# Optimization experiments

Hardware: AMD Instinct MI355X
Metric: run time of the kernel (lower is better)

## Reference

```python
import jax, jax.numpy as jnp
import numpy as np

B, S, E, H = 4, 2048, 1024, 16
D = E // H  # head dim = 64


def setup_inputs() -> dict:
    key = jax.random.key(0)
    ks = jax.random.split(key, 9)
    s_in = 1.0 / np.sqrt(E)
    return {
        "x": jax.random.normal(ks[0], (B, S, E), dtype=jnp.float32),
        # stacked per-head projection weights, acting as x @ W + b
        "Wq": jax.random.normal(ks[1], (H, E, D), dtype=jnp.float32) * s_in,
        "bq": jax.random.normal(ks[2], (H, D), dtype=jnp.float32) * 0.01,
        "Wk": jax.random.normal(ks[3], (H, E, D), dtype=jnp.float32) * s_in,
        "bk": jax.random.normal(ks[4], (H, D), dtype=jnp.float32) * 0.01,
        "Wv": jax.random.normal(ks[5], (H, E, D), dtype=jnp.float32) * s_in,
        "bv": jax.random.normal(ks[6], (H, D), dtype=jnp.float32) * 0.01,
        "Wo": jax.random.normal(ks[7], (E, E), dtype=jnp.float32) * s_in,
        "bo": jax.random.normal(ks[8], (E,), dtype=jnp.float32) * 0.01,
    }


def reference(x, Wq, bq, Wk, bk, Wv, bv, Wo, bo):
    # Batched per-head projections (equivalent to the per-head nn.Linear loop)
    q = jnp.einsum("bse,hed->bhsd", x, Wq) + bq[None, :, None, :]
    k = jnp.einsum("bse,hed->bhsd", x, Wk) + bk[None, :, None, :]
    v = jnp.einsum("bse,hed->bhsd", x, Wv) + bv[None, :, None, :]
    scale = 1.0 / jnp.sqrt(jnp.asarray(D, dtype=x.dtype))
    scores = jnp.einsum("bhsd,bhtd->bhst", q, k) * scale  # [B,H,S,S]
    attn = jax.nn.softmax(scores, axis=-1)
    ctx = jnp.einsum("bhst,bhtd->bhsd", attn, v)  # [B,H,S,D]
    # torch.cat over heads along last dim -> [B,S,H*D]=[B,S,E]
    ctx = jnp.transpose(ctx, (0, 2, 1, 3)).reshape(x.shape[0], x.shape[1], E)
    return ctx @ Wo + bo
```

## Files before the change

### kernel.cpp

```cpp
#include <hip/hip_runtime.h>
#include <math.h>

#define B_ 4
#define S_ 2048
#define E_ 1024
#define H_ 16
#define D_ 64
#define BH_ (B_ * H_)

#define SCALE_LOG2E 0.18033688011112042f

typedef short short8 __attribute__((ext_vector_type(8)));
typedef float f32x4 __attribute__((ext_vector_type(4)));
typedef float f32x16 __attribute__((ext_vector_type(16)));

static __device__ __forceinline__ unsigned short f2bf(float f) {
    unsigned int u = __float_as_uint(f);
    unsigned int r = (u + 0x7fffu + ((u >> 16) & 1u)) >> 16;
    return (unsigned short)r;
}

static __device__ __forceinline__ unsigned int pack_bf16_trunc(float hi, float lo) {
    return __builtin_amdgcn_perm(__float_as_uint(hi), __float_as_uint(lo), 0x07060302u);
}

static __device__ __forceinline__ void gl_lds16(const unsigned short* g, unsigned short* l) {
    __builtin_amdgcn_global_load_lds(
        (const __attribute__((address_space(1))) unsigned int*)g,
        (__attribute__((address_space(3))) unsigned int*)l, 16, 0, 0);
}


__global__ __launch_bounds__(256) void xcvt_kernel(
    const float* __restrict__ x, unsigned short* __restrict__ Xb)
{
    size_t i = ((size_t)blockIdx.x * 256 + threadIdx.x) * 8;
    float4 a = *(const float4*)&x[i];
    float4 b = *(const float4*)&x[i + 4];
    ushort4 u0, u1;
    u0.x = f2bf(a.x); u0.y = f2bf(a.y); u0.z = f2bf(a.z); u0.w = f2bf(a.w);
    u1.x = f2bf(b.x); u1.y = f2bf(b.y); u1.z = f2bf(b.z); u1.w = f2bf(b.w);
    *(ushort4*)&Xb[i]     = u0;
    *(ushort4*)&Xb[i + 4] = u1;
}

__global__ __launch_bounds__(256) void wtrans_qkv_kernel(
    const float* __restrict__ Wq, const float* __restrict__ Wk,
    const float* __restrict__ Wv, unsigned short* __restrict__ Wt)
{
    __shared__ float t[32][33];
    const int tx = threadIdx.x & 31, ty = threadIdx.x >> 5;
    const int r0 = blockIdx.x * 32, c0 = blockIdx.y * 32;
    const int z = blockIdx.z, mtx = z >> 4, h = z & 15;
    const float* s = (mtx == 0 ? Wq : (mtx == 1 ? Wk : Wv)) + (size_t)h * E_ * D_;
    const float scale = (mtx == 0) ? SCALE_LOG2E : 1.0f;
    unsigned short* d = Wt + (size_t)mtx * E_ * E_ + (size_t)h * D_ * E_;
#pragma unroll
    for (int i = 0; i < 4; ++i)
        t[ty + i * 8][tx] = s[(size_t)(r0 + ty + i * 8) * D_ + c0 + tx];
    __syncthreads();
#pragma unroll
    for (int i = 0; i < 4; ++i)
        d[(size_t)(c0 + ty + i * 8) * E_ + r0 + tx] = f2bf(t[tx][ty + i * 8] * scale);
}

__global__ __launch_bounds__(256) void wtrans_kernel(
    const float* __restrict__ src, unsigned short* __restrict__ dst, int R, int C)
{
    __shared__ float t[32][33];
    const int tx = threadIdx.x & 31, ty = threadIdx.x >> 5;
    const int r0 = blockIdx.x * 32, c0 = blockIdx.y * 32;
#pragma unroll
    for (int i = 0; i < 4; ++i)
        t[ty + i * 8][tx] = src[(size_t)(r0 + ty + i * 8) * C + c0 + tx];
    __syncthreads();
#pragma unroll
    for (int i = 0; i < 4; ++i)
        dst[(size_t)(c0 + ty + i * 8) * R + r0 + tx] = f2bf(t[tx][ty + i * 8]);
}

__global__ __launch_bounds__(256, 4) void qkv_gemm_kernel(
    const unsigned short* __restrict__ Xb, const unsigned short* __restrict__ Wt,
    const float* __restrict__ bq, const float* __restrict__ bk,
    const float* __restrict__ bv,
    unsigned short* __restrict__ Qh, unsigned short* __restrict__ Kh,
    unsigned short* __restrict__ Vth)
{
    __shared__ unsigned short As[2][128 * 32];
    __shared__ unsigned short Bs[2][128 * 32];
    const int tid = threadIdx.x;
    const int lane = tid & 63, wid = tid >> 6;
    const int quad = lane >> 4, lc = lane & 15;
    const int wm = wid >> 1, wn = wid & 1;
    const int m0 = blockIdx.y * 128, n0 = blockIdx.x * 128;
    const int srow = lane >> 2;
    const int sch  = (((lane & 3) ^ ((lane >> 2) & 3) ^ ((lane >> 4) & 3))) * 8;
    const int swzr = (lc & 3) ^ ((lc >> 2) & 3);

    f32x4 acc[4][4];
#pragma unroll
    for (int mt = 0; mt < 4; ++mt)
#pragma unroll
        for (int nt = 0; nt < 4; ++nt)
            acc[mt][nt] = (f32x4){0.f, 0.f, 0.f, 0.f};

#pragma unroll
    for (int i = 0; i < 2; ++i) {
        int rw = wid * 32 + i * 16;
        gl_lds16(&Xb[(size_t)(m0 + rw + srow) * E_ + sch], &As[0][rw * 32]);
        gl_lds16(&Wt[(size_t)(n0 + rw + srow) * E_ + sch], &Bs[0][rw * 32]);
    }
    __syncthreads();

    for (int k0 = 0; k0 < E_; k0 += 32) {
        const int cur = (k0 >> 5) & 1;
        if (k0 + 32 < E_) {
#pragma unroll
            for (int i = 0; i < 2; ++i) {
                int rw = wid * 32 + i * 16;
                gl_lds16(&Xb[(size_t)(m0 + rw + srow) * E_ + k0 + 32 + sch], &As[cur ^ 1][rw * 32]);
                gl_lds16(&Wt[(size_t)(n0 + rw + srow) * E_ + k0 + 32 + sch], &Bs[cur ^ 1][rw * 32]);
            }
        }
        short8 a[4], bfr[4];
#pragma unroll
        for (int mt = 0; mt < 4; ++mt)
            a[mt] = *(const short8*)&As[cur][(wm * 64 + mt * 16 + lc) * 32 +
                                            ((quad ^ swzr) << 3)];
#pragma unroll
        for (int nt = 0; nt < 4; ++nt)
            bfr[nt] = *(const short8*)&Bs[cur][(wn * 64 + nt * 16 + lc) * 32 +
                                              ((quad ^ swzr) << 3)];
#pragma unroll
        for (int mt = 0; mt < 4; ++mt)
#pragma unroll
            for (int nt = 0; nt < 4; ++nt)
                acc[mt][nt] = __builtin_amdgcn_mfma_f32_16x16x32_bf16(
                    a[mt], bfr[nt], acc[mt][nt], 0, 0, 0);
        __syncthreads();
    }

    const int nb = n0 + wn * 64;
    const int mtx = nb >> 10;
    const int h = (nb >> 6) & 15;
    const int sg0 = m0 + wm * 64;
    const int bb_ = sg0 >> 11;
    const int bhv = bb_ * H_ + h;
    if (mtx < 2) {
        const float bsc = (mtx == 0) ? SCALE_LOG2E : 1.0f;
        const float* bias = (mtx == 0 ? bq : bk) + h * D_;
        unsigned short* Out = (mtx == 0) ? Qh : Kh;
        const size_t obase = (size_t)bhv * (S_ / 32) * 2048;
#pragma unroll
        for (int nt = 0; nt < 4; ++nt) {
            int d = nt * 16 + lc;
            int hi_ = (lc >> 3) & 1, j = lc & 7;
            float bb = bias[d] * bsc;
#pragma unroll
            for (int mt = 0; mt < 4; ++mt)
#pragma unroll
                for (int r = 0; r < 4; ++r) {
                    int ss = (sg0 + mt * 16 + quad * 4 + r) & (S_ - 1);
                    Out[obase + ((size_t)(ss >> 5) * 4 + nt) * 512 +
                        ((ss & 31) * 2 + hi_) * 8 + j] = f2bf(acc[mt][nt][r] + bb);
                }
        }
    } else {
        const float* bias = bv + h * D_;
        const size_t obase = (size_t)bhv * (S_ / 64) * 4096;
        const int t64 = (sg0 & (S_ - 1)) >> 6;
        const int hi_ = quad >> 1, j0 = (quad & 1) * 4;
#pragma unroll
        for (int nt = 0; nt < 4; ++nt) {
            int d = nt * 16 + lc;
            int dsub = d >> 5, l31d = d & 31;
            float bb = bias[d];
#pragma unroll
            for (int mt = 0; mt < 4; ++mt) {
                ushort4 u;
                u.x = f2bf(acc[mt][nt][0] + bb);
                u.y = f2bf(acc[mt][nt][1] + bb);
                u.z = f2bf(acc[mt][nt][2] + bb);
                u.w = f2bf(acc[mt][nt][3] + bb);
                *(ushort4*)&Vth[obase + ((size_t)t64 * 8 + mt * 2 + dsub) * 512 +
                                (l31d * 2 + hi_) * 8 + j0] = u;
            }
        }
    }
}

__global__ __launch_bounds__(512, 4) void attn_kernel(
    const unsigned short* __restrict__ Qh, const unsigned short* __restrict__ Kh,
    const unsigned short* __restrict__ Vth, unsigned short* __restrict__ Ch)
{
    __shared__ unsigned short ks[3][8 * 512];
    __shared__ unsigned short vt[3][8 * 512];
    const int tid = threadIdx.x;
    const int lane = tid & 63, wid = tid >> 6;
    const int l31 = lane & 31, hi = lane >> 5;
    const int bh = blockIdx.x, b = bh >> 4, h = bh & 15;
    const int q0 = blockIdx.y * 256;
    const size_t gbase = (size_t)bh * (S_ / 32) * 2048;
    const int rdoff = (l31 * 2 + hi) * 8;
    const int ldoff = lane * 8;

    short8 qf[4];
    {
        const int t32 = (q0 >> 5) + wid;
#pragma unroll
        for (int kc = 0; kc < 4; ++kc)
            qf[kc] = *(const short8*)&Qh[gbase + ((size_t)t32 * 4 + kc) * 512 + rdoff];
    }

#pragma unroll
    for (int tt = 0; tt < 2; ++tt) {
        gl_lds16(&Kh[gbase + ((size_t)(tt * 2 + (wid >> 2)) * 4 + (wid & 3)) * 512 + ldoff],
                 &ks[tt][wid * 512]);
        gl_lds16(&Vth[gbase + ((size_t)tt * 8 + wid) * 512 + ldoff],
                 &vt[tt][wid * 512]);
    }
    __syncthreads();

    f32x16 ctx[2];
    float lsum = 0.f;
#pragma unroll
    for (int i = 0; i < 16; ++i) { ctx[0][i] = 0.f; ctx[1][i] = 0.f; }

    f32x16 stH;
#pragma unroll
    for (int i = 0; i < 16; ++i) stH[i] = 0.f;
#pragma unroll
    for (int kc = 0; kc < 4; ++kc) {
        short8 kf = *(const short8*)&ks[0][kc * 512 + rdoff];
        stH = __builtin_amdgcn_mfma_f32_32x32x16_bf16(kf, qf[kc], stH, 0, 0, 0);
    }

    auto smpv = [&](const f32x16& ST, int buf, int KB) {
#pragma unroll
        for (int ks16 = 0; ks16 < 2; ++ks16) {
            float e0 = __builtin_amdgcn_exp2f(ST[8 * ks16 + 0]);
            float e1 = __builtin_amdgcn_exp2f(ST[8 * ks16 + 1]);
            float e2 = __builtin_amdgcn_exp2f(ST[8 * ks16 + 2]);
            float e3 = __builtin_amdgcn_exp2f(ST[8 * ks16 + 3]);
            float e4 = __builtin_amdgcn_exp2f(ST[8 * ks16 + 4]);
            float e5 = __builtin_amdgcn_exp2f(ST[8 * ks16 + 5]);
            float e6 = __builtin_amdgcn_exp2f(ST[8 * ks16 + 6]);
            float e7 = __builtin_amdgcn_exp2f(ST[8 * ks16 + 7]);
            lsum += ((e0 + e1) + (e2 + e3)) + ((e4 + e5) + (e6 + e7));
            unsigned int w0 = pack_bf16_trunc(e1, e0);
            unsigned int w1 = pack_bf16_trunc(e3, e2);
            unsigned int w2 = pack_bf16_trunc(e5, e4);
            unsigned int w3 = pack_bf16_trunc(e7, e6);
            asm("v_permlane32_swap_b32 %0, %1" : "+v"(w0), "+v"(w2));
            asm("v_permlane32_swap_b32 %0, %1" : "+v"(w1), "+v"(w3));
            union { unsigned int u[4]; short8 s; } pu;
            pu.u[0] = w0; pu.u[1] = w1; pu.u[2] = w2; pu.u[3] = w3;
            const short8 pf = pu.s;
#pragma unroll
            for (int dsub = 0; dsub < 2; ++dsub) {
                short8 vf = *(const short8*)&vt[buf][((KB * 2 + ks16) * 2 + dsub) * 512 + rdoff];
                ctx[dsub] = __builtin_amdgcn_mfma_f32_32x32x16_bf16(
                    pf, vf, ctx[dsub], 0, 0, 0);
            }
        }
    };

    const int NT = S_ / 64;
    for (int t = 0; t < NT; ++t) {
        const int cur = t % 3, nxt = (t + 1) % 3, stg = (t + 2) % 3;
        if (t + 2 < NT) {
            gl_lds16(&Kh[gbase + ((size_t)((t + 2) * 2 + (wid >> 2)) * 4 + (wid & 3)) * 512 + ldoff],
                     &ks[stg][wid * 512]);
            gl_lds16(&Vth[gbase + ((size_t)(t + 2) * 8 + wid) * 512 + ldoff],
                     &vt[stg][wid * 512]);
        }

        f32x16 stN;
#pragma unroll
        for (int i = 0; i < 16; ++i) stN[i] = 0.f;
        __builtin_amdgcn_s_setprio(1);
#pragma unroll
        for (int kc = 0; kc < 4; ++kc) {
            short8 kf = *(const short8*)&ks[cur][(4 + kc) * 512 + rdoff];
            stN = __builtin_amdgcn_mfma_f32_32x32x16_bf16(kf, qf[kc], stN, 0, 0, 0);
        }
        __builtin_amdgcn_s_setprio(0);
        smpv(stH, cur, 0);
        stH = stN;

#pragma unroll
        for (int i = 0; i < 16; ++i) stN[i] = 0.f;
        if (t + 1 < NT) {
            __builtin_amdgcn_s_setprio(1);
#pragma unroll
            for (int kc = 0; kc < 4; ++kc) {
                short8 kf = *(const short8*)&ks[nxt][kc * 512 + rdoff];
                stN = __builtin_amdgcn_mfma_f32_32x32x16_bf16(kf, qf[kc], stN, 0, 0, 0);
            }
            __builtin_amdgcn_s_setprio(0);
        }
        smpv(stH, cur, 1);
        stH = stN;

        __syncthreads();
    }

    float* lsh = (float*)&ks[0][0];
    {
        float a = lsum, bx = lsum;
        asm("v_permlane32_swap_b32 %0, %1" : "+v"(a), "+v"(bx));
        float ltot = lsum + (hi ? a : bx);
        if (hi == 0) lsh[wid * 32 + l31] = ltot;
    }
    __syncthreads();
#pragma unroll
    for (int r = 0; r < 16; ++r) {
        int qr = (r & 3) + ((r >> 2) << 3) + hi * 4;
        float inv = 1.f / lsh[wid * 32 + qr];
        int q = q0 + wid * 32 + qr;
        size_t rowbase = ((size_t)b * S_ + q) * E_ + h * D_;
        Ch[rowbase + l31]      = f2bf(ctx[0][r] * inv);
        Ch[rowbase + 32 + l31] = f2bf(ctx[1][r] * inv);
    }
}

__global__ __launch_bounds__(256, 4) void out_proj_kernel(
    const unsigned short* __restrict__ Ch, const unsigned short* __restrict__ Wot,
    const float* __restrict__ bo, float* __restrict__ out)
{
    __shared__ unsigned short As[2][128 * 32];
    __shared__ unsigned short Bs[2][128 * 32];
    const int tid = threadIdx.x;
    const int lane = tid & 63, wid = tid >> 6;
    const int quad = lane >> 4, lc = lane & 15;
    const int wm = wid >> 1, wn = wid & 1;
    const int m0 = blockIdx.y * 128, n0 = blockIdx.x * 128;
    const int srow = lane >> 2;
    const int sch  = (((lane & 3) ^ ((lane >> 2) & 3) ^ ((lane >> 4) & 3))) * 8;
    const int swzr = (lc & 3) ^ ((lc >> 2) & 3);

    f32x4 acc[4][4];
#pragma unroll
    for (int mt = 0; mt < 4; ++mt)
#pragma unroll
        for (int nt = 0; nt < 4; ++nt)
            acc[mt][nt] = (f32x4){0.f, 0.f, 0.f, 0.f};

#pragma unroll
    for (int i = 0; i < 2; ++i) {
        int rw = wid * 32 + i * 16;
        gl_lds16(&Ch[(size_t)(m0 + rw + srow) * E_ + sch], &As[0][rw * 32]);
        gl_lds16(&Wot[(size_t)(n0 + rw + srow) * E_ + sch], &Bs[0][rw * 32]);
    }
    __syncthreads();

    for (int k0 = 0; k0 < E_; k0 += 32) {
        const int cur = (k0 >> 5) & 1;
        if (k0 + 32 < E_) {
#pragma unroll
            for (int i = 0; i < 2; ++i) {
                int rw = wid * 32 + i * 16;
                gl_lds16(&Ch[(size_t)(m0 + rw + srow) * E_ + k0 + 32 + sch], &As[cur ^ 1][rw * 32]);
                gl_lds16(&Wot[(size_t)(n0 + rw + srow) * E_ + k0 + 32 + sch], &Bs[cur ^ 1][rw * 32]);
            }
        }
        short8 a[4], bfr[4];
#pragma unroll
        for (int mt = 0; mt < 4; ++mt)
            a[mt] = *(const short8*)&As[cur][(wm * 64 + mt * 16 + lc) * 32 +
                                            ((quad ^ swzr) << 3)];
#pragma unroll
        for (int nt = 0; nt < 4; ++nt)
            bfr[nt] = *(const short8*)&Bs[cur][(wn * 64 + nt * 16 + lc) * 32 +
                                              ((quad ^ swzr) << 3)];
#pragma unroll
        for (int mt = 0; mt < 4; ++mt)
#pragma unroll
            for (int nt = 0; nt < 4; ++nt)
                acc[mt][nt] = __builtin_amdgcn_mfma_f32_16x16x32_bf16(
                    a[mt], bfr[nt], acc[mt][nt], 0, 0, 0);
        __syncthreads();
    }

#pragma unroll
    for (int mt = 0; mt < 4; ++mt)
#pragma unroll
        for (int nt = 0; nt < 4; ++nt) {
            int n = n0 + wn * 64 + nt * 16 + lc;
            float bb = bo[n];
#pragma unroll
            for (int r = 0; r < 4; ++r) {
                int row = m0 + wm * 64 + mt * 16 + quad * 4 + r;
                out[(size_t)row * E_ + n] = acc[mt][nt][r] + bb;
            }
        }
}

extern "C" void kernel_launch(void* const* d_in, const int* in_sizes, int n_in,
                              void* d_out, int out_size, void* d_ws, size_t ws_size,
                              hipStream_t stream)
{
    const float* x  = (const float*)d_in[0];
    const float* Wq = (const float*)d_in[1];
    const float* bq = (const float*)d_in[2];
    const float* Wk = (const float*)d_in[3];
    const float* bk = (const float*)d_in[4];
    const float* Wv = (const float*)d_in[5];
    const float* bv = (const float*)d_in[6];
    const float* Wo = (const float*)d_in[7];
    const float* bo = (const float*)d_in[8];
    (void)in_sizes; (void)n_in; (void)out_size; (void)ws_size;

    const size_t N = (size_t)BH_ * S_ * D_;
    unsigned short* Wt  = (unsigned short*)d_ws;
    unsigned short* Wot = Wt + (size_t)3072 * 1024;
    unsigned short* Xb  = Wot + (size_t)1024 * 1024;
    unsigned short* Qh  = Xb + N;
    unsigned short* Kh  = Qh + N;
    unsigned short* Vth = Kh + N;
    unsigned short* Ch  = Vth + N;

    xcvt_kernel<<<dim3(4096), 256, 0, stream>>>(x, Xb);
    wtrans_qkv_kernel<<<dim3(32, 2, 48), 256, 0, stream>>>(Wq, Wk, Wv, Wt);
    wtrans_kernel<<<dim3(32, 32, 1), 256, 0, stream>>>(Wo, Wot, E_, E_);

    qkv_gemm_kernel<<<dim3(24, 64), 256, 0, stream>>>(Xb, Wt, bq, bk, bv, Qh, Kh, Vth);
    attn_kernel<<<dim3(64, 8), 512, 0, stream>>>(Qh, Kh, Vth, Ch);
    out_proj_kernel<<<dim3(8, 64), 256, 0, stream>>>(Ch, Wot, bo, (float*)d_out);
}
```

Baseline: 276.8 us.

## Merge prep kernels into one launch and repack GEMM LDS tiles with XOR swizzle

The three preprocessing kernels (x to bf16 conversion, QKV weight transpose, Wo transpose) are merged into one launch that picks its job from the block index, removing two launch gaps. Both GEMM kernels change their LDS tile layout from 128x32 rows to 64x64 rows, each holding two logical rows, with a new XOR swizzle on the 16-byte chunks. The goal is fewer bank conflicts on the MFMA fragment reads and more contiguous global-to-LDS loads. The new address math is intricate, and a wrong mapping would silently corrupt results.

```diff
diff --git a/kernel.cpp b/kernel.cpp
--- a/kernel.cpp
+++ b/kernel.cpp
@@ -31,52 +31,53 @@
 }
 
 
-__global__ __launch_bounds__(256) void xcvt_kernel(
-    const float* __restrict__ x, unsigned short* __restrict__ Xb)
+__global__ __launch_bounds__(256) void prep_kernel(
+    const float* __restrict__ x, const float* __restrict__ Wq,
+    const float* __restrict__ Wk, const float* __restrict__ Wv,
+    const float* __restrict__ Wo,
+    unsigned short* __restrict__ Xb, unsigned short* __restrict__ Wt,
+    unsigned short* __restrict__ Wot)
 {
-    size_t i = ((size_t)blockIdx.x * 256 + threadIdx.x) * 8;
-    float4 a = *(const float4*)&x[i];
-    float4 b = *(const float4*)&x[i + 4];
-    ushort4 u0, u1;
-    u0.x = f2bf(a.x); u0.y = f2bf(a.y); u0.z = f2bf(a.z); u0.w = f2bf(a.w);
-    u1.x = f2bf(b.x); u1.y = f2bf(b.y); u1.z = f2bf(b.z); u1.w = f2bf(b.w);
-    *(ushort4*)&Xb[i]     = u0;
-    *(ushort4*)&Xb[i + 4] = u1;
-}
-
-__global__ __launch_bounds__(256) void wtrans_qkv_kernel(
-    const float* __restrict__ Wq, const float* __restrict__ Wk,
-    const float* __restrict__ Wv, unsigned short* __restrict__ Wt)
-{
+    const int bid = blockIdx.x;
+    if (bid < 4096) {
+        size_t i = ((size_t)bid * 256 + threadIdx.x) * 8;
+        float4 a = *(const float4*)&x[i];
+        float4 b = *(const float4*)&x[i + 4];
+        ushort4 u0, u1;
+        u0.x = f2bf(a.x); u0.y = f2bf(a.y); u0.z = f2bf(a.z); u0.w = f2bf(a.w);
+        u1.x = f2bf(b.x); u1.y = f2bf(b.y); u1.z = f2bf(b.z); u1.w = f2bf(b.w);
+        *(ushort4*)&Xb[i]     = u0;
+        *(ushort4*)&Xb[i + 4] = u1;
+        return;
+    }
     __shared__ float t[32][33];
     const int tx = threadIdx.x & 31, ty = threadIdx.x >> 5;
-    const int r0 = blockIdx.x * 32, c0 = blockIdx.y * 32;
-    const int z = blockIdx.z, mtx = z >> 4, h = z & 15;
-    const float* s = (mtx == 0 ? Wq : (mtx == 1 ? Wk : Wv)) + (size_t)h * E_ * D_;
-    const float scale = (mtx == 0) ? SCALE_LOG2E : 1.0f;
-    unsigned short* d = Wt + (size_t)mtx * E_ * E_ + (size_t)h * D_ * E_;
-#pragma unroll
-    for (int i = 0; i < 4; ++i)
-        t[ty + i * 8][tx] = s[(size_t)(r0 + ty + i * 8) * D_ + c0 + tx];
-    __syncthreads();
-#pragma unroll
-    for (int i = 0; i < 4; ++i)
-        d[(size_t)(c0 + ty + i * 8) * E_ + r0 + tx] = f2bf(t[tx][ty + i * 8] * scale);
-}
-
-__global__ __launch_bounds__(256) void wtrans_kernel(
-    const float* __restrict__ src, unsigned short* __restrict__ dst, int R, int C)
-{
-    __shared__ float t[32][33];
-    const int tx = threadIdx.x & 31, ty = threadIdx.x >> 5;
-    const int r0 = blockIdx.x * 32, c0 = blockIdx.y * 32;
-#pragma unroll
-    for (int i = 0; i < 4; ++i)
-        t[ty + i * 8][tx] = src[(size_t)(r0 + ty + i * 8) * C + c0 + tx];
-    __syncthreads();
-#pragma unroll
-    for (int i = 0; i < 4; ++i)
-        dst[(size_t)(c0 + ty + i * 8) * R + r0 + tx] = f2bf(t[tx][ty + i * 8]);
+    if (bid < 7168) {
+        const int idx = bid - 4096;
+        const int z = idx >> 6, rem = idx & 63;
+        const int r0 = (rem & 31) * 32, c0 = (rem >> 5) * 32;
+        const int mtx = z >> 4, h = z & 15;
+        const float* s = (mtx == 0 ? Wq : (mtx == 1 ? Wk : Wv)) + (size_t)h * E_ * D_;
+        const float scale = (mtx == 0) ? SCALE_LOG2E : 1.0f;
+        unsigned short* d = Wt + (size_t)mtx * E_ * E_ + (size_t)h * D_ * E_;
+#pragma unroll
+        for (int i = 0; i < 4; ++i)
+            t[ty + i * 8][tx] = s[(size_t)(r0 + ty + i * 8) * D_ + c0 + tx];
+        __syncthreads();
+#pragma unroll
+        for (int i = 0; i < 4; ++i)
+            d[(size_t)(c0 + ty + i * 8) * E_ + r0 + tx] = f2bf(t[tx][ty + i * 8] * scale);
+    } else {
+        const int idx = bid - 7168;
+        const int r0 = (idx & 31) * 32, c0 = (idx >> 5) * 32;
+#pragma unroll
+        for (int i = 0; i < 4; ++i)
+            t[ty + i * 8][tx] = Wo[(size_t)(r0 + ty + i * 8) * E_ + c0 + tx];
+        __syncthreads();
+#pragma unroll
+        for (int i = 0; i < 4; ++i)
+            Wot[(size_t)(c0 + ty + i * 8) * E_ + r0 + tx] = f2bf(t[tx][ty + i * 8]);
+    }
 }
 
 __global__ __launch_bounds__(256, 4) void qkv_gemm_kernel(
@@ -86,16 +87,18 @@
     unsigned short* __restrict__ Qh, unsigned short* __restrict__ Kh,
     unsigned short* __restrict__ Vth)
 {
-    __shared__ unsigned short As[2][128 * 32];
-    __shared__ unsigned short Bs[2][128 * 32];
+    __shared__ unsigned short As[2][64 * 64];
+    __shared__ unsigned short Bs[2][64 * 64];
     const int tid = threadIdx.x;
     const int lane = tid & 63, wid = tid >> 6;
     const int quad = lane >> 4, lc = lane & 15;
     const int wm = wid >> 1, wn = wid & 1;
     const int m0 = blockIdx.y * 128, n0 = blockIdx.x * 128;
-    const int srow = lane >> 2;
-    const int sch  = (((lane & 3) ^ ((lane >> 2) & 3) ^ ((lane >> 4) & 3))) * 8;
-    const int swzr = (lc & 3) ^ ((lc >> 2) & 3);
+    const int l3 = lane >> 3;
+    const int cs = (lane & 7) ^ l3;
+    const int mloc = 2 * l3 + (cs >> 2);
+    const int koff = (cs & 3) * 8;
+    const int rdbase = (lc >> 1) * 64 + (((((lc & 1) << 2) | quad) ^ ((lc >> 1) & 7)) << 3);
 
     f32x4 acc[4][4];
 #pragma unroll
@@ -106,9 +109,9 @@
 
 #pragma unroll
     for (int i = 0; i < 2; ++i) {
-        int rw = wid * 32 + i * 16;
-        gl_lds16(&Xb[(size_t)(m0 + rw + srow) * E_ + sch], &As[0][rw * 32]);
-        gl_lds16(&Wt[(size_t)(n0 + rw + srow) * E_ + sch], &Bs[0][rw * 32]);
+        int Rb = wid * 16 + i * 8;
+        gl_lds16(&Xb[(size_t)(m0 + Rb * 2 + mloc) * E_ + koff], &As[0][Rb * 64]);
+        gl_lds16(&Wt[(size_t)(n0 + Rb * 2 + mloc) * E_ + koff], &Bs[0][Rb * 64]);
     }
     __syncthreads();
 
@@ -117,20 +120,20 @@
         if (k0 + 32 < E_) {
 #pragma unroll
             for (int i = 0; i < 2; ++i) {
-                int rw = wid * 32 + i * 16;
-                gl_lds16(&Xb[(size_t)(m0 + rw + srow) * E_ + k0 + 32 + sch], &As[cur ^ 1][rw * 32]);
-                gl_lds16(&Wt[(size_t)(n0 + rw + srow) * E_ + k0 + 32 + sch], &Bs[cur ^ 1][rw * 32]);
+                int Rb = wid * 16 + i * 8;
+                gl_lds16(&Xb[(size_t)(m0 + Rb * 2 + mloc) * E_ + k0 + 32 + koff],
+                         &As[cur ^ 1][Rb * 64]);
+                gl_lds16(&Wt[(size_t)(n0 + Rb * 2 + mloc) * E_ + k0 + 32 + koff],
+                         &Bs[cur ^ 1][Rb * 64]);
             }
         }
         short8 a[4], bfr[4];
 #pragma unroll
         for (int mt = 0; mt < 4; ++mt)
-            a[mt] = *(const short8*)&As[cur][(wm * 64 + mt * 16 + lc) * 32 +
-                                            ((quad ^ swzr) << 3)];
+            a[mt] = *(const short8*)&As[cur][(wm * 32 + mt * 8) * 64 + rdbase];
 #pragma unroll
         for (int nt = 0; nt < 4; ++nt)
-            bfr[nt] = *(const short8*)&Bs[cur][(wn * 64 + nt * 16 + lc) * 32 +
-                                              ((quad ^ swzr) << 3)];
+            bfr[nt] = *(const short8*)&Bs[cur][(wn * 32 + nt * 8) * 64 + rdbase];
 #pragma unroll
         for (int mt = 0; mt < 4; ++mt)
 #pragma unroll
@@ -328,16 +331,18 @@
     const unsigned short* __restrict__ Ch, const unsigned short* __restrict__ Wot,
     const float* __restrict__ bo, float* __restrict__ out)
 {
-    __shared__ unsigned short As[2][128 * 32];
-    __shared__ unsigned short Bs[2][128 * 32];
+    __shared__ unsigned short As[2][64 * 64];
+    __shared__ unsigned short Bs[2][64 * 64];
     const int tid = threadIdx.x;
     const int lane = tid & 63, wid = tid >> 6;
     const int quad = lane >> 4, lc = lane & 15;
     const int wm = wid >> 1, wn = wid & 1;
     const int m0 = blockIdx.y * 128, n0 = blockIdx.x * 128;
-    const int srow = lane >> 2;
-    const int sch  = (((lane & 3) ^ ((lane >> 2) & 3) ^ ((lane >> 4) & 3))) * 8;
-    const int swzr = (lc & 3) ^ ((lc >> 2) & 3);
+    const int l3 = lane >> 3;
+    const int cs = (lane & 7) ^ l3;
+    const int mloc = 2 * l3 + (cs >> 2);
+    const int koff = (cs & 3) * 8;
+    const int rdbase = (lc >> 1) * 64 + (((((lc & 1) << 2) | quad) ^ ((lc >> 1) & 7)) << 3);
 
     f32x4 acc[4][4];
 #pragma unroll
@@ -348,9 +353,9 @@
 
 #pragma unroll
     for (int i = 0; i < 2; ++i) {
-        int rw = wid * 32 + i * 16;
-        gl_lds16(&Ch[(size_t)(m0 + rw + srow) * E_ + sch], &As[0][rw * 32]);
-        gl_lds16(&Wot[(size_t)(n0 + rw + srow) * E_ + sch], &Bs[0][rw * 32]);
+        int Rb = wid * 16 + i * 8;
+        gl_lds16(&Ch[(size_t)(m0 + Rb * 2 + mloc) * E_ + koff], &As[0][Rb * 64]);
+        gl_lds16(&Wot[(size_t)(n0 + Rb * 2 + mloc) * E_ + koff], &Bs[0][Rb * 64]);
     }
     __syncthreads();
 
@@ -359,20 +364,20 @@
         if (k0 + 32 < E_) {
 #pragma unroll
             for (int i = 0; i < 2; ++i) {
-                int rw = wid * 32 + i * 16;
-                gl_lds16(&Ch[(size_t)(m0 + rw + srow) * E_ + k0 + 32 + sch], &As[cur ^ 1][rw * 32]);
-                gl_lds16(&Wot[(size_t)(n0 + rw + srow) * E_ + k0 + 32 + sch], &Bs[cur ^ 1][rw * 32]);
+                int Rb = wid * 16 + i * 8;
+                gl_lds16(&Ch[(size_t)(m0 + Rb * 2 + mloc) * E_ + k0 + 32 + koff],
+                         &As[cur ^ 1][Rb * 64]);
+                gl_lds16(&Wot[(size_t)(n0 + Rb * 2 + mloc) * E_ + k0 + 32 + koff],
+                         &Bs[cur ^ 1][Rb * 64]);
             }
         }
         short8 a[4], bfr[4];
 #pragma unroll
         for (int mt = 0; mt < 4; ++mt)
-            a[mt] = *(const short8*)&As[cur][(wm * 64 + mt * 16 + lc) * 32 +
-                                            ((quad ^ swzr) << 3)];
+            a[mt] = *(const short8*)&As[cur][(wm * 32 + mt * 8) * 64 + rdbase];
 #pragma unroll
         for (int nt = 0; nt < 4; ++nt)
-            bfr[nt] = *(const short8*)&Bs[cur][(wn * 64 + nt * 16 + lc) * 32 +
-                                              ((quad ^ swzr) << 3)];
+            bfr[nt] = *(const short8*)&Bs[cur][(wn * 32 + nt * 8) * 64 + rdbase];
 #pragma unroll
         for (int mt = 0; mt < 4; ++mt)
 #pragma unroll
@@ -420,10 +425,7 @@
     unsigned short* Vth = Kh + N;
     unsigned short* Ch  = Vth + N;
 
-    xcvt_kernel<<<dim3(4096), 256, 0, stream>>>(x, Xb);
-    wtrans_qkv_kernel<<<dim3(32, 2, 48), 256, 0, stream>>>(Wq, Wk, Wv, Wt);
-    wtrans_kernel<<<dim3(32, 32, 1), 256, 0, stream>>>(Wo, Wot, E_, E_);
-
+    prep_kernel<<<dim3(8192), 256, 0, stream>>>(x, Wq, Wk, Wv, Wo, Xb, Wt, Wot);
     qkv_gemm_kernel<<<dim3(24, 64), 256, 0, stream>>>(Xb, Wt, bq, bk, bv, Qh, Kh, Vth);
     attn_kernel<<<dim3(64, 8), 512, 0, stream>>>(Qh, Kh, Vth, Ch);
     out_proj_kernel<<<dim3(8, 64), 256, 0, stream>>>(Ch, Wot, bo, (float*)d_out);
```

New measurement: 268.4 us. 3.0% less time.
